# Kernel tuning notes

Hardware: AMD Instinct MI355X
Metric: run time of the kernel (lower is better)

## Reference

```python
import jax, jax.numpy as jnp
import numpy as np

C_, A_, B_ = 1, 128, 128          # image_size
H, Z, T, N = 512, 128, 16, 32     # h_dim, z_dim, steps, attention grid
EPS = 1e-8
BATCH = 256
PATCH = C_ * N * N                # read/write patch size (C_=1)
IN_ENC = 2 * PATCH + H


def gru_cell(x, h, W_ih, W_hh, b_ih, b_hh):
    gi = x @ W_ih.T + b_ih
    gh = h @ W_hh.T + b_hh
    i_r, i_z, i_n = jnp.split(gi, 3, axis=-1)
    h_r, h_z, h_n = jnp.split(gh, 3, axis=-1)
    r = jax.nn.sigmoid(i_r + h_r)
    z = jax.nn.sigmoid(i_z + h_z)
    n = jnp.tanh(i_n + r * h_n)
    return (1.0 - z) * n + z * h


def filterbank(gt, delta, two_sigma_sq, num_pixels):
    # gt, delta: [b,1]; two_sigma_sq: [b,1,1]
    g = 0.5 * (num_pixels + 1) * (gt + 1.0)                       # [b,1]
    grid = jnp.arange(N, dtype=jnp.float32) - 0.5 * (N - 1)       # [N]
    mu = g + grid[None, :] * delta                                # [b,N]
    pix = jnp.arange(num_pixels, dtype=jnp.float32)               # [P]
    F = jnp.exp(-(pix[None, None, :] - mu[:, :, None]) ** 2 / two_sigma_sq)
    return F / jnp.maximum(F.sum(axis=-1, keepdims=True), EPS)    # [b,N,P]


def get_filterbanks(h_dec, W_attn, b_attn):
    p = h_dec @ W_attn.T + b_attn                                 # [b,5]
    gt_x, gt_y, log_ss, log_dt, log_g = [p[:, i:i + 1] for i in range(5)]
    two_sigma_sq = (2.0 * jnp.exp(log_ss))[:, :, None]            # [b,1,1]
    delta = (max(A_, B_) - 1) * jnp.exp(log_dt) / (N - 1)         # [b,1]
    gamma = jnp.exp(log_g)                                        # [b,1]
    F_x = filterbank(gt_x, delta, two_sigma_sq, A_)               # [b,N,A]
    F_y = filterbank(gt_y, delta, two_sigma_sq, B_)               # [b,N,B]
    return F_x, F_y, gamma


def draw_forward(x, eps, W_ih_enc, W_hh_enc, b_ih_enc, b_hh_enc,
                 W_ih_dec, W_hh_dec, b_ih_dec, b_hh_dec,
                 W_mu, b_mu, W_ls, b_ls, W_wr, b_wr,
                 W_ra, b_ra, W_wa, b_wa):
    b = x.shape[0]
    xf = x.reshape(b, -1)                                         # [b, A*B]
    reconsts0 = jnp.zeros_like(xf)
    h0 = jnp.zeros((b, H), dtype=xf.dtype)

    def step(carry, eps_t):
        reconsts, h_enc, h_dec = carry
        # NOTE: faithful to original: reconsts[-1] is last batch row, broadcast
        x_hat = xf - jax.nn.sigmoid(reconsts[-1])
        # ---- read with attention ----
        F_x, F_y, gamma = get_filterbanks(h_dec, W_ra, b_ra)
        F_x_t = jnp.swapaxes(F_x, -1, -2)                         # [b,A,N]
        img = xf.reshape(b, A_, B_)
        img_hat = x_hat.reshape(b, A_, B_)
        x_attn = (F_y @ img @ F_x_t).reshape(b, -1)               # [b,N*N]
        xh_attn = (F_y @ img_hat @ F_x_t).reshape(b, -1)
        r = gamma * jnp.concatenate([x_attn, xh_attn], axis=1)    # [b,2*N*N]
        # ---- encoder GRU ----
        h_enc = gru_cell(jnp.concatenate([r, h_dec], axis=1), h_enc,
                         W_ih_enc, W_hh_enc, b_ih_enc, b_hh_enc)
        # ---- sample z ~ Q ----
        mu = h_enc @ W_mu.T + b_mu
        sigma = jnp.exp(h_enc @ W_ls.T + b_ls)
        z = mu + eps_t * sigma
        # ---- decoder GRU ----
        h_dec = gru_cell(z, h_dec, W_ih_dec, W_hh_dec, b_ih_dec, b_hh_dec)
        # ---- write with attention ----
        F_xw, F_yw, gamma_w = get_filterbanks(h_dec, W_wa, b_wa)
        w = (h_dec @ W_wr.T + b_wr).reshape(b, N, N)
        wr = (jnp.swapaxes(F_yw, -1, -2) @ w @ F_xw).reshape(b, -1) / gamma_w
        return (reconsts + wr, h_enc, h_dec), None

    (reconsts, _, _), _ = jax.lax.scan(step, (reconsts0, h0, h0), eps)
    return jax.nn.sigmoid(reconsts).reshape(-1, C_, A_, B_)


def setup_inputs() -> dict:
    key = jax.random.key(0)
    ks = jax.random.split(key, 24)
    s = 0.02
    inp = {
        "x": jax.random.uniform(ks[0], (BATCH, C_, A_, B_), jnp.float32),
        "eps": jax.random.normal(ks[1], (T, BATCH, Z), jnp.float32),
        "W_ih_enc": jax.random.normal(ks[2], (3 * H, IN_ENC), jnp.float32) * s,
        "W_hh_enc": jax.random.normal(ks[3], (3 * H, H), jnp.float32) * s,
        "b_ih_enc": jnp.zeros((3 * H,), jnp.float32),
        "b_hh_enc": jnp.zeros((3 * H,), jnp.float32),
        "W_ih_dec": jax.random.normal(ks[4], (3 * H, Z), jnp.float32) * s,
        "W_hh_dec": jax.random.normal(ks[5], (3 * H, H), jnp.float32) * s,
        "b_ih_dec": jnp.zeros((3 * H,), jnp.float32),
        "b_hh_dec": jnp.zeros((3 * H,), jnp.float32),
        "W_mu": jax.random.normal(ks[6], (Z, H), jnp.float32) * s,
        "b_mu": jnp.zeros((Z,), jnp.float32),
        "W_ls": jax.random.normal(ks[7], (Z, H), jnp.float32) * s,
        "b_ls": jnp.zeros((Z,), jnp.float32),
        "W_wr": jax.random.normal(ks[8], (PATCH, H), jnp.float32) * s,
        "b_wr": jnp.zeros((PATCH,), jnp.float32),
        "W_ra": jax.random.normal(ks[9], (5, H), jnp.float32) * s,
        "b_ra": jnp.zeros((5,), jnp.float32),
        "W_wa": jax.random.normal(ks[10], (5, H), jnp.float32) * s,
        "b_wa": jnp.zeros((5,), jnp.float32),
    }
    return inp


def reference(x, eps, W_ih_enc, W_hh_enc, b_ih_enc, b_hh_enc,
              W_ih_dec, W_hh_dec, b_ih_dec, b_hh_dec,
              W_mu, b_mu, W_ls, b_ls, W_wr, b_wr,
              W_ra, b_ra, W_wa, b_wa):
    return draw_forward(x, eps, W_ih_enc, W_hh_enc, b_ih_enc, b_hh_enc,
                        W_ih_dec, W_hh_dec, b_ih_dec, b_hh_dec,
                        W_mu, b_mu, W_ls, b_ls, W_wr, b_wr,
                        W_ra, b_ra, W_wa, b_wa)
```

## Files before the change

kernel.cpp:

```cpp
#include <hip/hip_runtime.h>
#include <math.h>

#define BATCHN 256
#define HDIM 512
#define ZDIM 128
#define NGRID 32
#define ABDIM 128
#define IMGSZ 16384
#define ENCIN 2560
#define G3 1536
#define SLAB (BATCHN*G3)

typedef __attribute__((ext_vector_type(8))) short short8;
typedef __attribute__((ext_vector_type(4))) float f32x4;

__device__ __forceinline__ float sigmoidf_(float x){ return 1.0f/(1.0f+expf(-x)); }

__device__ __forceinline__ ushort f2bf_rne(float f){
    union{float f; uint u;} x; x.f=f;
    uint r = (x.u + 0x7FFFu + ((x.u>>16)&1u)) >> 16;
    return (ushort)r;
}
__device__ __forceinline__ float bf2f(ushort h){
    union{uint u; float f;} y; y.u = ((uint)h)<<16;
    return y.f;
}

__global__ void init_slast_k(float* __restrict__ s_last){
    int i = blockIdx.x*256 + threadIdx.x;
    s_last[i] = 0.5f;
}

__global__ void conv_wh_k(const float* __restrict__ W, ushort* __restrict__ Wh, int n4){
    int i = blockIdx.x*256 + threadIdx.x;
    if(i>=n4) return;
    float4 v = ((const float4*)W)[i];
    ushort4 hv;
    hv.x=f2bf_rne(v.x); hv.y=f2bf_rne(v.y); hv.z=f2bf_rne(v.z); hv.w=f2bf_rne(v.w);
    ((ushort4*)Wh)[i] = hv;
}

__device__ __forceinline__ void attn_params_dev512(const float* __restrict__ h,
        const float* __restrict__ W, const float* __restrict__ bvec,
        float* red5, float* pp, int tid){
    float accp[5];
    #pragma unroll
    for(int i=0;i<5;i++) accp[i]=0.f;
    for(int k=tid;k<HDIM;k+=512){
        float hv = h[k];
        #pragma unroll
        for(int i=0;i<5;i++) accp[i] += hv*W[i*HDIM+k];
    }
    int wv = tid>>6;
    #pragma unroll
    for(int i=0;i<5;i++){
        float a = accp[i];
        #pragma unroll
        for(int o=32;o>0;o>>=1) a += __shfl_down(a,o);
        if((tid&63)==0) red5[i*8+wv]=a;
    }
    __syncthreads();
    if(tid<5){
        float s = bvec[tid];
        #pragma unroll
        for(int w2=0;w2<8;w2++) s += red5[tid*8+w2];
        pp[tid]=s;
    }
    __syncthreads();
}

__device__ __forceinline__ void fill_fb_T(float* fxT, float* fyT, const float* pp, int tid){
    float gx = 64.5f*(pp[0]+1.0f);
    float gy = 64.5f*(pp[1]+1.0f);
    float tss = 2.0f*expf(pp[2]);
    float delta = (127.0f/31.0f)*expf(pp[3]);
    int rr = tid>>3;
    int q  = tid&7;
    int j  = rr&31;
    bool isY = rr>=32;
    float mu = (isY?gy:gx) + ((float)j-15.5f)*delta;
    float v[16]; float s=0.f;
    #pragma unroll
    for(int i=0;i<16;i++){
        float d = (float)(q*16+i)-mu;
        float e = expf(-d*d/tss);
        v[i]=e; s+=e;
    }
    s += __shfl_xor(s,1); s += __shfl_xor(s,2); s += __shfl_xor(s,4);
    float inv = 1.0f/fmaxf(s,1e-8f);
    float* dst = isY? fyT : fxT;
    #pragma unroll
    for(int i=0;i<16;i++) dst[(q*16+i)*32 + j] = v[i]*inv;
    __syncthreads();
}

__device__ __forceinline__ void fill_fb_R(float (*fx)[ABDIM+1], float (*fy)[ABDIM+1], const float* pp, int tid){
    float gx = 64.5f*(pp[0]+1.0f);
    float gy = 64.5f*(pp[1]+1.0f);
    float tss = 2.0f*expf(pp[2]);
    float delta = (127.0f/31.0f)*expf(pp[3]);
    int rr = tid>>3;
    int q  = tid&7;
    int j  = rr&31;
    bool isY = rr>=32;
    float mu = (isY?gy:gx) + ((float)j-15.5f)*delta;
    float v[16]; float s=0.f;
    #pragma unroll
    for(int i=0;i<16;i++){
        float d = (float)(q*16+i)-mu;
        float e = expf(-d*d/tss);
        v[i]=e; s+=e;
    }
    s += __shfl_xor(s,1); s += __shfl_xor(s,2); s += __shfl_xor(s,4);
    float inv = 1.0f/fmaxf(s,1e-8f);
    float* rowp = isY? &fy[j][0] : &fx[j][0];
    #pragma unroll
    for(int i=0;i<16;i++) rowp[q*16+i] = v[i]*inv;
    __syncthreads();
}

__global__ __launch_bounds__(512) void read_attn_k(const float* __restrict__ xf, const float* __restrict__ s_last,
        const float* __restrict__ hdec, const ushort* __restrict__ Hd_h, const ushort* __restrict__ Hd_l,
        const float* __restrict__ W_ra, const float* __restrict__ b_ra,
        ushort* __restrict__ Eh, ushort* __restrict__ El){
    __shared__ float smem[4096 + 8256 + 48];
    float* sFxT = smem;
    float* sFyT = smem + 4096;
    float* tmp  = smem + 4096;
    float* red5 = smem + 4096 + 8256;
    float* pp   = red5 + 40;
    int bb = blockIdx.x; int tid = threadIdx.x;
    const float* h = hdec + bb*HDIM;
    attn_params_dev512(h, W_ra, b_ra, red5, pp, tid);
    float gamma = expf(pp[4]);
    fill_fb_T(sFxT, sFyT, pp, tid);

    const float* img = xf + (size_t)bb*IMGSZ;
    int c = tid & 127;
    int jg = tid >> 7;
    float acc0[8], accS[8];
    #pragma unroll
    for(int i=0;i<8;i++){ acc0[i]=0.f; accS[i]=0.f; }
    for(int k=0;k<ABDIM;k++){
        float s  = img[k*ABDIM + c];
        float sl = s_last[k*ABDIM + c];
        float4 f0 = *(const float4*)&sFyT[k*32 + jg*8];
        float4 f1 = *(const float4*)&sFyT[k*32 + jg*8 + 4];
        acc0[0]+=f0.x*s;  acc0[1]+=f0.y*s;  acc0[2]+=f0.z*s;  acc0[3]+=f0.w*s;
        acc0[4]+=f1.x*s;  acc0[5]+=f1.y*s;  acc0[6]+=f1.z*s;  acc0[7]+=f1.w*s;
        accS[0]+=f0.x*sl; accS[1]+=f0.y*sl; accS[2]+=f0.z*sl; accS[3]+=f0.w*sl;
        accS[4]+=f1.x*sl; accS[5]+=f1.y*sl; accS[6]+=f1.z*sl; accS[7]+=f1.w*sl;
    }
    __syncthreads();
    #pragma unroll
    for(int i=0;i<8;i++){
        int j = jg*8+i;
        tmp[0*32*129 + j*129 + c] = acc0[i];
        tmp[1*32*129 + j*129 + c] = acc0[i] - accS[i];
    }
    __syncthreads();
    {
        int i4 = tid & 7;
        int j  = (tid>>3) & 31;
        int p  = tid >> 8;
        float a0=0.f,a1=0.f,a2=0.f,a3=0.f;
        for(int cc=0; cc<ABDIM; cc++){
            float tv = tmp[p*32*129 + j*129 + cc];
            float4 fx = *(const float4*)&sFxT[cc*32 + i4*4];
            a0 += tv*fx.x; a1 += tv*fx.y; a2 += tv*fx.z; a3 += tv*fx.w;
        }
        float ov[4] = {gamma*a0, gamma*a1, gamma*a2, gamma*a3};
        ushort4 oh, ol; ushort hq;
        hq=f2bf_rne(ov[0]); oh.x=hq; ol.x=f2bf_rne(ov[0]-bf2f(hq));
        hq=f2bf_rne(ov[1]); oh.y=hq; ol.y=f2bf_rne(ov[1]-bf2f(hq));
        hq=f2bf_rne(ov[2]); oh.z=hq; ol.z=f2bf_rne(ov[2]-bf2f(hq));
        hq=f2bf_rne(ov[3]); oh.w=hq; ol.w=f2bf_rne(ov[3]-bf2f(hq));
        size_t off = (size_t)bb*ENCIN + p*1024 + j*NGRID + i4*4;
        *(ushort4*)(Eh + off) = oh;
        *(ushort4*)(El + off) = ol;
    }
    {
        int i = tid;
        Eh[(size_t)bb*ENCIN + 2048 + i] = Hd_h[(size_t)bb*HDIM + i];
        El[(size_t)bb*ENCIN + 2048 + i] = Hd_l[(size_t)bb*HDIM + i];
    }
}

__device__ void gemm_one(const ushort* __restrict__ Agh, const ushort* __restrict__ Agl,
        const ushort* __restrict__ Wh,
        int K, int k0, int kiters, int row0, int col0, int Nn, float* __restrict__ Out,
        ushort* AH, ushort* AL, ushort* BH, int tid){
    int lane = tid&63, w = tid>>6;
    int m0 = (w>>1)*32, n0 = (w&1)*32;
    int fr = lane&15, kq = (lane>>4)*8;
    int sr = tid>>2, sq = (tid&3)*16;
    f32x4 acc[2][2];
    #pragma unroll
    for(int i=0;i<2;i++)
        #pragma unroll
        for(int j=0;j<2;j++) acc[i][j]=(f32x4){0.f,0.f,0.f,0.f};
    for(int it=0; it<kiters; ++it){
        int kb = k0 + it*64;
        size_t aoff = (size_t)(row0+sr)*K + kb + sq;
        size_t boff = (size_t)(col0+sr)*K + kb + sq;
        uint4 ah0 = *(const uint4*)(Agh + aoff);
        uint4 ah1 = *(const uint4*)(Agh + aoff + 8);
        uint4 al0 = *(const uint4*)(Agl + aoff);
        uint4 al1 = *(const uint4*)(Agl + aoff + 8);
        uint4 bh0 = *(const uint4*)(Wh + boff);
        uint4 bh1 = *(const uint4*)(Wh + boff + 8);
        __syncthreads();
        *(uint4*)&AH[sr*72 + sq]     = ah0;
        *(uint4*)&AH[sr*72 + sq + 8] = ah1;
        *(uint4*)&AL[sr*72 + sq]     = al0;
        *(uint4*)&AL[sr*72 + sq + 8] = al1;
        *(uint4*)&BH[sr*72 + sq]     = bh0;
        *(uint4*)&BH[sr*72 + sq + 8] = bh1;
        __syncthreads();
        #pragma unroll
        for(int ks=0; ks<2; ks++){
            int kk = ks*32 + kq;
            short8 a_h[2], a_l[2], b_h[2];
            #pragma unroll
            for(int mf=0;mf<2;mf++){
                a_h[mf] = *(short8*)&AH[(m0+mf*16+fr)*72 + kk];
                a_l[mf] = *(short8*)&AL[(m0+mf*16+fr)*72 + kk];
            }
            #pragma unroll
            for(int nf=0;nf<2;nf++)
                b_h[nf] = *(short8*)&BH[(n0+nf*16+fr)*72 + kk];
            #pragma unroll
            for(int mf=0;mf<2;mf++)
                #pragma unroll
                for(int nf=0;nf<2;nf++){
                    acc[mf][nf] = __builtin_amdgcn_mfma_f32_16x16x32_bf16(a_h[mf], b_h[nf], acc[mf][nf], 0,0,0);
                    acc[mf][nf] = __builtin_amdgcn_mfma_f32_16x16x32_bf16(a_l[mf], b_h[nf], acc[mf][nf], 0,0,0);
                }
        }
    }
    int crow = (lane>>4)*4, ccol = lane&15;
    #pragma unroll
    for(int mf=0;mf<2;mf++)
        #pragma unroll
        for(int nf=0;nf<2;nf++)
            #pragma unroll
            for(int r=0;r<4;r++)
                Out[(size_t)(row0+m0+mf*16+crow+r)*Nn + col0+n0+nf*16+ccol] = acc[mf][nf][r];
}

__global__ __launch_bounds__(256) void gemm3_k(
        const ushort* __restrict__ Eh, const ushort* __restrict__ El,
        const ushort* __restrict__ Wie_h,
        const ushort* __restrict__ He_h, const ushort* __restrict__ He_l,
        const ushort* __restrict__ Whe_h,
        const ushort* __restrict__ Hd_h, const ushort* __restrict__ Hd_l,
        const ushort* __restrict__ Whd_h,
        float* __restrict__ Pi, float* __restrict__ Ph, float* __restrict__ Ph2){
    __shared__ ushort AH[64*72], AL[64*72], BH[64*72];
    int job = blockIdx.x, tid = threadIdx.x;
    if(job < 384){
        int tile = job % 96, s = job / 96;
        gemm_one(Eh, El, Wie_h, ENCIN, s*640, 10,
                 (tile/24)*64, (tile%24)*64, G3, Pi + (size_t)s*SLAB, AH, AL, BH, tid);
    } else if(job < 480){
        int tile = job - 384;
        gemm_one(He_h, He_l, Whe_h, HDIM, 0, 8,
                 (tile/24)*64, (tile%24)*64, G3, Ph, AH, AL, BH, tid);
    } else {
        int tile = job - 480;
        gemm_one(Hd_h, Hd_l, Whd_h, HDIM, 0, 8,
                 (tile/24)*64, (tile%24)*64, G3, Ph2, AH, AL, BH, tid);
    }
}

__global__ __launch_bounds__(256) void gemm_wr_k(
        const ushort* __restrict__ Hd_h, const ushort* __restrict__ Hd_l,
        const ushort* __restrict__ Wwr_h,
        float* __restrict__ Pw){
    __shared__ ushort AH[64*72], AL[64*72], BH[64*72];
    int tid = threadIdx.x;
    int r0 = blockIdx.y*64, c0 = blockIdx.x*64, s = blockIdx.z;
    gemm_one(Hd_h, Hd_l, Wwr_h, HDIM, s*128, 2, r0, c0, 1024,
             Pw + (size_t)s*BATCHN*1024, AH, AL, BH, tid);
}

__global__ __launch_bounds__(512) void combine_z_k(const float* __restrict__ Pi, const float* __restrict__ Ph,
        const float* __restrict__ bi, const float* __restrict__ bh,
        float* __restrict__ h, ushort* __restrict__ Hh, ushort* __restrict__ Hl,
        const float* __restrict__ Wmu, const float* __restrict__ bmu,
        const float* __restrict__ Wls, const float* __restrict__ bls,
        const float* __restrict__ eps_t, ushort* __restrict__ Zh, ushort* __restrict__ Zl){
    __shared__ float hs[HDIM];
    int bb = blockIdx.x, tid = threadIdx.x;
    int j = tid;
    float gi_r=bi[j], gi_z=bi[512+j], gi_n=bi[1024+j];
    float gh_r=bh[j], gh_z=bh[512+j], gh_n=bh[1024+j];
    #pragma unroll
    for(int s=0;s<4;s++){
        size_t base = (size_t)s*SLAB + (size_t)bb*G3 + j;
        gi_r += Pi[base]; gi_z += Pi[base+512]; gi_n += Pi[base+1024];
    }
    {
        size_t base = (size_t)bb*G3 + j;
        gh_r += Ph[base]; gh_z += Ph[base+512]; gh_n += Ph[base+1024];
    }
    float r = sigmoidf_(gi_r + gh_r);
    float z = sigmoidf_(gi_z + gh_z);
    float n = tanhf(gi_n + r*gh_n);
    size_t hoff = (size_t)bb*HDIM + j;
    float hn = (1.f - z)*n + z*h[hoff];
    h[hoff] = hn; hs[j] = hn;
    ushort hh = f2bf_rne(hn);
    Hh[hoff] = hh; Hl[hoff] = f2bf_rne(hn - bf2f(hh));
    __syncthreads();
    {
        int wv = tid>>6, lane = tid&63;
        const float4* hs4 = (const float4*)hs;
        float4 h0 = hs4[lane*2];
        float4 h1 = hs4[lane*2+1];
        #pragma unroll 4
        for(int it=0; it<16; ++it){
            int jo = wv*16 + it;
            const float4* wm = (const float4*)(Wmu + (size_t)jo*HDIM);
            const float4* wl = (const float4*)(Wls + (size_t)jo*HDIM);
            float4 m0=wm[lane*2], m1=wm[lane*2+1];
            float4 l0=wl[lane*2], l1=wl[lane*2+1];
            float am  = h0.x*m0.x+h0.y*m0.y+h0.z*m0.z+h0.w*m0.w
                      + h1.x*m1.x+h1.y*m1.y+h1.z*m1.z+h1.w*m1.w;
            float al_ = h0.x*l0.x+h0.y*l0.y+h0.z*l0.z+h0.w*l0.w
                      + h1.x*l1.x+h1.y*l1.y+h1.z*l1.z+h1.w*l1.w;
            #pragma unroll
            for(int o=32;o>0;o>>=1){ am += __shfl_down(am,o); al_ += __shfl_down(al_,o); }
            if(lane==0){
                float mu = am + bmu[jo];
                float sg = expf(al_ + bls[jo]);
                float zv = mu + eps_t[(size_t)bb*ZDIM + jo]*sg;
                ushort zh = f2bf_rne(zv);
                Zh[(size_t)bb*ZDIM + jo] = zh;
                Zl[(size_t)bb*ZDIM + jo] = f2bf_rne(zv - bf2f(zh));
            }
        }
    }
}

__global__ __launch_bounds__(256) void deci_combine_k(
        const ushort* __restrict__ Zh, const ushort* __restrict__ Zl,
        const ushort* __restrict__ Wid_h,
        const float* __restrict__ Ph2, const float* __restrict__ bi, const float* __restrict__ bh,
        float* __restrict__ h, ushort* __restrict__ Hh, ushort* __restrict__ Hl){
    __shared__ ushort AH[64*72], AL[64*72], BH[64*72];
    int tid = threadIdx.x;
    int lane = tid&63, w = tid>>6;
    int m0 = (w>>1)*32, n0 = (w&1)*32;
    int fr = lane&15, kq = (lane>>4)*8;
    int sr = tid>>2, sq = (tid&3)*16;
    int row0 = blockIdx.y*64;
    int jcol0 = blockIdx.x*64;
    f32x4 acc[3][2][2];
    #pragma unroll
    for(int g=0;g<3;g++)
        #pragma unroll
        for(int i=0;i<2;i++)
            #pragma unroll
            for(int jj=0;jj<2;jj++) acc[g][i][jj]=(f32x4){0.f,0.f,0.f,0.f};
    for(int it=0; it<2; ++it){
        int kb = it*64;
        size_t aoff = (size_t)(row0+sr)*ZDIM + kb + sq;
        uint4 ah0 = *(const uint4*)(Zh + aoff);
        uint4 ah1 = *(const uint4*)(Zh + aoff + 8);
        uint4 al0 = *(const uint4*)(Zl + aoff);
        uint4 al1 = *(const uint4*)(Zl + aoff + 8);
        __syncthreads();
        *(uint4*)&AH[sr*72 + sq]     = ah0;
        *(uint4*)&AH[sr*72 + sq + 8] = ah1;
        *(uint4*)&AL[sr*72 + sq]     = al0;
        *(uint4*)&AL[sr*72 + sq + 8] = al1;
        for(int g=0; g<3; ++g){
            size_t boff = (size_t)(g*512 + jcol0 + sr)*ZDIM + kb + sq;
            uint4 bh0 = *(const uint4*)(Wid_h + boff);
            uint4 bh1 = *(const uint4*)(Wid_h + boff + 8);
            if(g>0) __syncthreads();
            *(uint4*)&BH[sr*72 + sq]     = bh0;
            *(uint4*)&BH[sr*72 + sq + 8] = bh1;
            __syncthreads();
            #pragma unroll
            for(int ks=0; ks<2; ks++){
                int kk = ks*32 + kq;
                short8 a_h[2], a_l[2], b_h[2];
                #pragma unroll
                for(int mf=0;mf<2;mf++){
                    a_h[mf] = *(short8*)&AH[(m0+mf*16+fr)*72 + kk];
                    a_l[mf] = *(short8*)&AL[(m0+mf*16+fr)*72 + kk];
                }
                #pragma unroll
                for(int nf=0;nf<2;nf++)
                    b_h[nf] = *(short8*)&BH[(n0+nf*16+fr)*72 + kk];
                #pragma unroll
                for(int mf=0;mf<2;mf++)
                    #pragma unroll
                    for(int nf=0;nf<2;nf++){
                        acc[g][mf][nf] = __builtin_amdgcn_mfma_f32_16x16x32_bf16(a_h[mf], b_h[nf], acc[g][mf][nf], 0,0,0);
                        acc[g][mf][nf] = __builtin_amdgcn_mfma_f32_16x16x32_bf16(a_l[mf], b_h[nf], acc[g][mf][nf], 0,0,0);
                    }
            }
        }
    }
    int crow = (lane>>4)*4, ccol = lane&15;
    #pragma unroll
    for(int mf=0;mf<2;mf++)
        #pragma unroll
        for(int nf=0;nf<2;nf++)
            #pragma unroll
            for(int r=0;r<4;r++){
                int row = row0 + m0 + mf*16 + crow + r;
                int col = jcol0 + n0 + nf*16 + ccol;
                size_t pbase = (size_t)row*G3 + col;
                float gi_r = acc[0][mf][nf][r] + bi[col];
                float gi_z = acc[1][mf][nf][r] + bi[512+col];
                float gi_n = acc[2][mf][nf][r] + bi[1024+col];
                float gh_r = Ph2[pbase]      + bh[col];
                float gh_z = Ph2[pbase+512]  + bh[512+col];
                float gh_n = Ph2[pbase+1024] + bh[1024+col];
                float rr = sigmoidf_(gi_r + gh_r);
                float zz = sigmoidf_(gi_z + gh_z);
                float nn = tanhf(gi_n + rr*gh_n);
                size_t idx = (size_t)row*HDIM + col;
                float hn = (1.f - zz)*nn + zz*h[idx];
                h[idx] = hn;
                ushort hh = f2bf_rne(hn);
                Hh[idx] = hh; Hl[idx] = f2bf_rne(hn - bf2f(hh));
            }
}

__global__ __launch_bounds__(512) void write_apply_k(const float* __restrict__ Pw, const float* __restrict__ b_wr,
        const float* __restrict__ hdec, const float* __restrict__ W_wa, const float* __restrict__ b_wa,
        float* __restrict__ rec, float* __restrict__ s_last){
    __shared__ float sFy[NGRID][ABDIM+1];
    __shared__ float sFx[NGRID][ABDIM+1];
    __shared__ float sw[NGRID][36];
    __shared__ float t[ABDIM][36];
    __shared__ float red5[40];
    __shared__ float pp[8];
    int bb = blockIdx.x, tid = threadIdx.x;
    const float* h = hdec + bb*HDIM;
    attn_params_dev512(h, W_wa, b_wa, red5, pp, tid);
    float invg = expf(-pp[4]);
    fill_fb_R(sFx, sFy, pp, tid);
    for(int i=tid;i<NGRID*NGRID;i+=512){
        float a = b_wr[i];
        #pragma unroll
        for(int s=0;s<4;s++) a += Pw[((size_t)s*BATCHN + bb)*1024 + i];
        sw[i>>5][i&31] = a;
    }
    __syncthreads();
    {
        int p = tid>>2, iq = tid&3;
        float a[8];
        #pragma unroll
        for(int i=0;i<8;i++) a[i]=0.f;
        for(int j=0;j<NGRID;j++){
            float fy = sFy[j][p];
            float4 w0 = *(const float4*)&sw[j][iq*8];
            float4 w1 = *(const float4*)&sw[j][iq*8+4];
            a[0]+=fy*w0.x; a[1]+=fy*w0.y; a[2]+=fy*w0.z; a[3]+=fy*w0.w;
            a[4]+=fy*w1.x; a[5]+=fy*w1.y; a[6]+=fy*w1.z; a[7]+=fy*w1.w;
        }
        float4 o0; o0.x=a[0];o0.y=a[1];o0.z=a[2];o0.w=a[3];
        float4 o1; o1.x=a[4];o1.y=a[5];o1.z=a[6];o1.w=a[7];
        *(float4*)&t[p][iq*8]   = o0;
        *(float4*)&t[p][iq*8+4] = o1;
    }
    __syncthreads();
    {
        int q = tid&127, pg = tid>>7;
        float fxc[32];
        #pragma unroll
        for(int i=0;i<32;i++) fxc[i] = sFx[i][q];
        for(int pi=0; pi<32; pi++){
            int p = pg*32 + pi;
            float acc = 0.f;
            #pragma unroll
            for(int i4=0;i4<8;i4++){
                float4 tv = *(const float4*)&t[p][i4*4];
                acc += tv.x*fxc[i4*4] + tv.y*fxc[i4*4+1] + tv.z*fxc[i4*4+2] + tv.w*fxc[i4*4+3];
            }
            size_t off = (size_t)bb*IMGSZ + p*ABDIM + q;
            float nv = rec[off] + acc*invg;
            rec[off] = nv;
            if(bb==BATCHN-1) s_last[p*ABDIM + q] = sigmoidf_(nv);
        }
    }
}

__global__ void sigmoid_all_k(float* __restrict__ rec){
    int i = blockIdx.x*256 + threadIdx.x;
    rec[i] = sigmoidf_(rec[i]);
}

extern "C" void kernel_launch(void* const* d_in, const int* in_sizes, int n_in,
                              void* d_out, int out_size, void* d_ws, size_t ws_size,
                              hipStream_t stream) {
    const float* x        = (const float*)d_in[0];
    const float* eps      = (const float*)d_in[1];
    const float* W_ih_enc = (const float*)d_in[2];
    const float* W_hh_enc = (const float*)d_in[3];
    const float* b_ih_enc = (const float*)d_in[4];
    const float* b_hh_enc = (const float*)d_in[5];
    const float* W_ih_dec = (const float*)d_in[6];
    const float* W_hh_dec = (const float*)d_in[7];
    const float* b_ih_dec = (const float*)d_in[8];
    const float* b_hh_dec = (const float*)d_in[9];
    const float* W_mu     = (const float*)d_in[10];
    const float* b_mu     = (const float*)d_in[11];
    const float* W_ls     = (const float*)d_in[12];
    const float* b_ls     = (const float*)d_in[13];
    const float* W_wr     = (const float*)d_in[14];
    const float* b_wr     = (const float*)d_in[15];
    const float* W_ra     = (const float*)d_in[16];
    const float* b_ra     = (const float*)d_in[17];
    const float* W_wa     = (const float*)d_in[18];
    const float* b_wa     = (const float*)d_in[19];

    float* rec = (float*)d_out;

    float* ws = (float*)d_ws;
    float* h_enc  = ws;  ws += BATCHN*HDIM;
    float* h_dec  = ws;  ws += BATCHN*HDIM;
    float* s_last = ws;  ws += IMGSZ;
    float* Pi     = ws;  ws += (size_t)4*SLAB;
    float* Ph     = ws;  ws += (size_t)SLAB;
    float* Ph2    = ws;  ws += (size_t)SLAB;
    float* Pw     = ws;  ws += (size_t)4*BATCHN*1024;

    ushort* us = (ushort*)ws;
    ushort* Wie_h = us; us += 1536*2560;
    ushort* Whe_h = us; us += 1536*512;
    ushort* Whd_h = us; us += 1536*512;
    ushort* Wid_h = us; us += 1536*128;
    ushort* Wwr_h = us; us += 1024*512;
    ushort* Eh    = us; us += BATCHN*ENCIN;
    ushort* El    = us; us += BATCHN*ENCIN;
    ushort* He_h  = us; us += BATCHN*HDIM;
    ushort* He_l  = us; us += BATCHN*HDIM;
    ushort* Hd_h  = us; us += BATCHN*HDIM;
    ushort* Hd_l  = us; us += BATCHN*HDIM;
    ushort* Zh    = us; us += BATCHN*ZDIM;
    ushort* Zl    = us; us += BATCHN*ZDIM;

    hipMemsetAsync(rec,   0, (size_t)BATCHN*IMGSZ*sizeof(float), stream);
    hipMemsetAsync(h_enc, 0, (size_t)BATCHN*HDIM*sizeof(float), stream);
    hipMemsetAsync(h_dec, 0, (size_t)BATCHN*HDIM*sizeof(float), stream);
    hipMemsetAsync(He_h,  0, (size_t)BATCHN*HDIM*sizeof(ushort)*2, stream);
    hipMemsetAsync(Hd_h,  0, (size_t)BATCHN*HDIM*sizeof(ushort)*2, stream);
    init_slast_k<<<IMGSZ/256,256,0,stream>>>(s_last);

    conv_wh_k<<<(1536*2560/4+255)/256,256,0,stream>>>(W_ih_enc, Wie_h, 1536*2560/4);
    conv_wh_k<<<(1536*512/4+255)/256,256,0,stream>>>(W_hh_enc, Whe_h, 1536*512/4);
    conv_wh_k<<<(1536*512/4+255)/256,256,0,stream>>>(W_hh_dec, Whd_h, 1536*512/4);
    conv_wh_k<<<(1536*128/4+255)/256,256,0,stream>>>(W_ih_dec, Wid_h, 1536*128/4);
    conv_wh_k<<<(1024*512/4+255)/256,256,0,stream>>>(W_wr, Wwr_h, 1024*512/4);

    for(int t=0;t<16;t++){
        read_attn_k<<<BATCHN,512,0,stream>>>(x, s_last, h_dec, Hd_h, Hd_l, W_ra, b_ra, Eh, El);
        gemm3_k<<<576,256,0,stream>>>(Eh, El, Wie_h, He_h, He_l, Whe_h,
                                      Hd_h, Hd_l, Whd_h, Pi, Ph, Ph2);
        combine_z_k<<<BATCHN,512,0,stream>>>(Pi, Ph, b_ih_enc, b_hh_enc,
            h_enc, He_h, He_l, W_mu, b_mu, W_ls, b_ls, eps + (size_t)t*BATCHN*ZDIM, Zh, Zl);
        deci_combine_k<<<dim3(8,4),256,0,stream>>>(Zh, Zl, Wid_h, Ph2,
            b_ih_dec, b_hh_dec, h_dec, Hd_h, Hd_l);
        gemm_wr_k<<<dim3(16,4,4),256,0,stream>>>(Hd_h, Hd_l, Wwr_h, Pw);
        write_apply_k<<<BATCHN,512,0,stream>>>(Pw, b_wr, h_dec, W_wa, b_wa, rec, s_last);
    }
    sigmoid_all_k<<<BATCHN*IMGSZ/256,256,0,stream>>>(rec);
}
```

Measured before the change: 1.408 ms.

## Stage GEMM tiles with direct global-to-LDS loads and fold final sigmoid

The register-staged global loads in the GEMM helpers are replaced by global_load_lds direct copies into an XOR-swizzled LDS layout without padding, removing the register round trip and one barrier per K step (a trailing barrier is added instead). The final sigmoid pass over the whole output is folded into the last write_apply launch, saving one full read and write of the reconstruction buffer. The swizzle must match the MFMA fragment read pattern, and the direct LDS loads depend on wave-uniform destination addressing.

```diff
diff --git a/kernel.cpp b/kernel.cpp
--- a/kernel.cpp
+++ b/kernel.cpp
@@ -38,6 +38,25 @@
     ushort4 hv;
     hv.x=f2bf_rne(v.x); hv.y=f2bf_rne(v.y); hv.z=f2bf_rne(v.z); hv.w=f2bf_rne(v.w);
     ((ushort4*)Wh)[i] = hv;
+}
+
+__device__ __forceinline__ void stage_swz(const ushort* __restrict__ g, int K,
+        int grow0, int kb, ushort* lds, int tid){
+    int wv = tid>>6, lane = tid&63;
+    #pragma unroll
+    for(int q=0;q<2;q++){
+        int instr = wv*2 + q;
+        int rl = instr*8 + (lane>>3);
+        int sc = (lane&7) ^ (lane>>3);
+        const ushort* src = g + (size_t)(grow0+rl)*K + kb + sc*8;
+        ushort* dst = lds + instr*512;
+        __builtin_amdgcn_global_load_lds((const __attribute__((address_space(1))) void*)src,
+                                         (__attribute__((address_space(3))) void*)dst, 16, 0, 0);
+    }
+}
+
+__device__ __forceinline__ short8 lds_read_swz(const ushort* arr, int r, int slot){
+    return *(const short8*)&arr[r*64 + ((slot ^ (r&7))<<3)];
 }
 
 __device__ __forceinline__ void attn_params_dev512(const float* __restrict__ h,
@@ -192,8 +211,7 @@
         ushort* AH, ushort* AL, ushort* BH, int tid){
     int lane = tid&63, w = tid>>6;
     int m0 = (w>>1)*32, n0 = (w&1)*32;
-    int fr = lane&15, kq = (lane>>4)*8;
-    int sr = tid>>2, sq = (tid&3)*16;
+    int fr = lane&15, sl = lane>>4;
     f32x4 acc[2][2];
     #pragma unroll
     for(int i=0;i<2;i++)
@@ -201,34 +219,22 @@
         for(int j=0;j<2;j++) acc[i][j]=(f32x4){0.f,0.f,0.f,0.f};
     for(int it=0; it<kiters; ++it){
         int kb = k0 + it*64;
-        size_t aoff = (size_t)(row0+sr)*K + kb + sq;
-        size_t boff = (size_t)(col0+sr)*K + kb + sq;
-        uint4 ah0 = *(const uint4*)(Agh + aoff);
-        uint4 ah1 = *(const uint4*)(Agh + aoff + 8);
-        uint4 al0 = *(const uint4*)(Agl + aoff);
-        uint4 al1 = *(const uint4*)(Agl + aoff + 8);
-        uint4 bh0 = *(const uint4*)(Wh + boff);
-        uint4 bh1 = *(const uint4*)(Wh + boff + 8);
+        stage_swz(Agh, K, row0, kb, AH, tid);
+        stage_swz(Agl, K, row0, kb, AL, tid);
+        stage_swz(Wh,  K, col0, kb, BH, tid);
         __syncthreads();
-        *(uint4*)&AH[sr*72 + sq]     = ah0;
-        *(uint4*)&AH[sr*72 + sq + 8] = ah1;
-        *(uint4*)&AL[sr*72 + sq]     = al0;
-        *(uint4*)&AL[sr*72 + sq + 8] = al1;
-        *(uint4*)&BH[sr*72 + sq]     = bh0;
-        *(uint4*)&BH[sr*72 + sq + 8] = bh1;
-        __syncthreads();
         #pragma unroll
         for(int ks=0; ks<2; ks++){
-            int kk = ks*32 + kq;
+            int slot = ks*4 + sl;
             short8 a_h[2], a_l[2], b_h[2];
             #pragma unroll
             for(int mf=0;mf<2;mf++){
-                a_h[mf] = *(short8*)&AH[(m0+mf*16+fr)*72 + kk];
-                a_l[mf] = *(short8*)&AL[(m0+mf*16+fr)*72 + kk];
+                a_h[mf] = lds_read_swz(AH, m0+mf*16+fr, slot);
+                a_l[mf] = lds_read_swz(AL, m0+mf*16+fr, slot);
             }
             #pragma unroll
             for(int nf=0;nf<2;nf++)
-                b_h[nf] = *(short8*)&BH[(n0+nf*16+fr)*72 + kk];
+                b_h[nf] = lds_read_swz(BH, n0+nf*16+fr, slot);
             #pragma unroll
             for(int mf=0;mf<2;mf++)
                 #pragma unroll
@@ -237,6 +243,7 @@
                     acc[mf][nf] = __builtin_amdgcn_mfma_f32_16x16x32_bf16(a_l[mf], b_h[nf], acc[mf][nf], 0,0,0);
                 }
         }
+        __syncthreads();
     }
     int crow = (lane>>4)*4, ccol = lane&15;
     #pragma unroll
@@ -256,7 +263,7 @@
         const ushort* __restrict__ Hd_h, const ushort* __restrict__ Hd_l,
         const ushort* __restrict__ Whd_h,
         float* __restrict__ Pi, float* __restrict__ Ph, float* __restrict__ Ph2){
-    __shared__ ushort AH[64*72], AL[64*72], BH[64*72];
+    __shared__ ushort AH[64*64], AL[64*64], BH[64*64];
     int job = blockIdx.x, tid = threadIdx.x;
     if(job < 384){
         int tile = job % 96, s = job / 96;
@@ -277,7 +284,7 @@
         const ushort* __restrict__ Hd_h, const ushort* __restrict__ Hd_l,
         const ushort* __restrict__ Wwr_h,
         float* __restrict__ Pw){
-    __shared__ ushort AH[64*72], AL[64*72], BH[64*72];
+    __shared__ ushort AH[64*64], AL[64*64], BH[64*64];
     int tid = threadIdx.x;
     int r0 = blockIdx.y*64, c0 = blockIdx.x*64, s = blockIdx.z;
     gemm_one(Hd_h, Hd_l, Wwr_h, HDIM, s*128, 2, r0, c0, 1024,
@@ -348,12 +355,11 @@
         const ushort* __restrict__ Wid_h,
         const float* __restrict__ Ph2, const float* __restrict__ bi, const float* __restrict__ bh,
         float* __restrict__ h, ushort* __restrict__ Hh, ushort* __restrict__ Hl){
-    __shared__ ushort AH[64*72], AL[64*72], BH[64*72];
+    __shared__ ushort AH[64*64], AL[64*64], BH[64*64];
     int tid = threadIdx.x;
     int lane = tid&63, w = tid>>6;
     int m0 = (w>>1)*32, n0 = (w&1)*32;
-    int fr = lane&15, kq = (lane>>4)*8;
-    int sr = tid>>2, sq = (tid&3)*16;
+    int fr = lane&15, sl = lane>>4;
     int row0 = blockIdx.y*64;
     int jcol0 = blockIdx.x*64;
     f32x4 acc[3][2][2];
@@ -365,36 +371,23 @@
             for(int jj=0;jj<2;jj++) acc[g][i][jj]=(f32x4){0.f,0.f,0.f,0.f};
     for(int it=0; it<2; ++it){
         int kb = it*64;
-        size_t aoff = (size_t)(row0+sr)*ZDIM + kb + sq;
-        uint4 ah0 = *(const uint4*)(Zh + aoff);
-        uint4 ah1 = *(const uint4*)(Zh + aoff + 8);
-        uint4 al0 = *(const uint4*)(Zl + aoff);
-        uint4 al1 = *(const uint4*)(Zl + aoff + 8);
-        __syncthreads();
-        *(uint4*)&AH[sr*72 + sq]     = ah0;
-        *(uint4*)&AH[sr*72 + sq + 8] = ah1;
-        *(uint4*)&AL[sr*72 + sq]     = al0;
-        *(uint4*)&AL[sr*72 + sq + 8] = al1;
+        stage_swz(Zh, ZDIM, row0, kb, AH, tid);
+        stage_swz(Zl, ZDIM, row0, kb, AL, tid);
         for(int g=0; g<3; ++g){
-            size_t boff = (size_t)(g*512 + jcol0 + sr)*ZDIM + kb + sq;
-            uint4 bh0 = *(const uint4*)(Wid_h + boff);
-            uint4 bh1 = *(const uint4*)(Wid_h + boff + 8);
-            if(g>0) __syncthreads();
-            *(uint4*)&BH[sr*72 + sq]     = bh0;
-            *(uint4*)&BH[sr*72 + sq + 8] = bh1;
+            stage_swz(Wid_h, ZDIM, g*512 + jcol0, kb, BH, tid);
             __syncthreads();
             #pragma unroll
             for(int ks=0; ks<2; ks++){
-                int kk = ks*32 + kq;
+                int slot = ks*4 + sl;
                 short8 a_h[2], a_l[2], b_h[2];
                 #pragma unroll
                 for(int mf=0;mf<2;mf++){
-                    a_h[mf] = *(short8*)&AH[(m0+mf*16+fr)*72 + kk];
-                    a_l[mf] = *(short8*)&AL[(m0+mf*16+fr)*72 + kk];
+                    a_h[mf] = lds_read_swz(AH, m0+mf*16+fr, slot);
+                    a_l[mf] = lds_read_swz(AL, m0+mf*16+fr, slot);
                 }
                 #pragma unroll
                 for(int nf=0;nf<2;nf++)
-                    b_h[nf] = *(short8*)&BH[(n0+nf*16+fr)*72 + kk];
+                    b_h[nf] = lds_read_swz(BH, n0+nf*16+fr, slot);
                 #pragma unroll
                 for(int mf=0;mf<2;mf++)
                     #pragma unroll
@@ -403,6 +396,7 @@
                         acc[g][mf][nf] = __builtin_amdgcn_mfma_f32_16x16x32_bf16(a_l[mf], b_h[nf], acc[g][mf][nf], 0,0,0);
                     }
             }
+            __syncthreads();
         }
     }
     int crow = (lane>>4)*4, ccol = lane&15;
@@ -434,7 +428,7 @@
 
 __global__ __launch_bounds__(512) void write_apply_k(const float* __restrict__ Pw, const float* __restrict__ b_wr,
         const float* __restrict__ hdec, const float* __restrict__ W_wa, const float* __restrict__ b_wa,
-        float* __restrict__ rec, float* __restrict__ s_last){
+        float* __restrict__ rec, float* __restrict__ s_last, int last){
     __shared__ float sFy[NGRID][ABDIM+1];
     __shared__ float sFx[NGRID][ABDIM+1];
     __shared__ float sw[NGRID][36];
@@ -486,15 +480,10 @@
             }
             size_t off = (size_t)bb*IMGSZ + p*ABDIM + q;
             float nv = rec[off] + acc*invg;
-            rec[off] = nv;
+            rec[off] = last ? sigmoidf_(nv) : nv;
             if(bb==BATCHN-1) s_last[p*ABDIM + q] = sigmoidf_(nv);
         }
     }
-}
-
-__global__ void sigmoid_all_k(float* __restrict__ rec){
-    int i = blockIdx.x*256 + threadIdx.x;
-    rec[i] = sigmoidf_(rec[i]);
 }
 
 extern "C" void kernel_launch(void* const* d_in, const int* in_sizes, int n_in,
@@ -569,7 +558,7 @@
         deci_combine_k<<<dim3(8,4),256,0,stream>>>(Zh, Zl, Wid_h, Ph2,
             b_ih_dec, b_hh_dec, h_dec, Hd_h, Hd_l);
         gemm_wr_k<<<dim3(16,4,4),256,0,stream>>>(Hd_h, Hd_l, Wwr_h, Pw);
-        write_apply_k<<<BATCHN,512,0,stream>>>(Pw, b_wr, h_dec, W_wa, b_wa, rec, s_last);
-    }
-    sigmoid_all_k<<<BATCHN*IMGSZ/256,256,0,stream>>>(rec);
-}
+        write_apply_k<<<BATCHN,512,0,stream>>>(Pw, b_wr, h_dec, W_wa, b_wa, rec, s_last,
+                                               (t==15)?1:0);
+    }
+}
```

Result: faster. 1.376 ms (-2.2%).
